# Kernel optimization log

Hardware: AMD Instinct MI355X
Metric: run time of the kernel (lower is better)

The kernel has to match this reference:

```python
import jax, jax.numpy as jnp
import numpy as np

E = 1024   # embed_dim
H = 16     # num_heads
D = E // H # head_dim = 64
HD2 = D // 2
B = 2
S = 2048


def setup_inputs() -> dict:
    key = jax.random.key(0)
    ks = jax.random.split(key, 12)
    def lin(k, fan_in, fan_out):
        # xavier-uniform-ish init, stored in [in, out] (jax) convention
        lim = float(np.sqrt(6.0 / (fan_in + fan_out)))
        return jax.random.uniform(k, (fan_in, fan_out), jnp.float32, -lim, lim)
    return {
        "query": jax.random.normal(ks[0], (B, S, E), jnp.float32),
        "xi_scale": jax.random.uniform(ks[1], (B,), jnp.float32),
        "Wq": lin(ks[2], E, E), "bq": jnp.zeros((E,), jnp.float32),
        "Wk": lin(ks[3], E, E), "bk": jnp.zeros((E,), jnp.float32),
        "Wv": lin(ks[4], E, E), "bv": jnp.zeros((E,), jnp.float32),
        "Wo": lin(ks[5], E, E), "bo": jnp.zeros((E,), jnp.float32),
        "enc_w1": lin(ks[6], 1, HD2), "enc_b1": jnp.zeros((HD2,), jnp.float32),
        "ln_g": jnp.ones((HD2,), jnp.float32), "ln_b": jnp.zeros((HD2,), jnp.float32),
        "enc_w2": lin(ks[7], HD2, D), "enc_b2": jnp.zeros((D,), jnp.float32),
        "scale_gating": jnp.ones((H,), jnp.float32),
    }


def reference(query, xi_scale, Wq, bq, Wk, bk, Wv, bv, Wo, bo,
              enc_w1, enc_b1, ln_g, ln_b, enc_w2, enc_b2, scale_gating):
    b, s, e = query.shape
    h, d = H, e // H
    # --- scale adaptation: xi -> Linear -> LayerNorm -> GELU -> Linear ---
    x = xi_scale[:, None] @ enc_w1 + enc_b1                  # [B, D/2]
    mu = x.mean(-1, keepdims=True)
    var = ((x - mu) ** 2).mean(-1, keepdims=True)
    x = (x - mu) / jnp.sqrt(var + 1e-5) * ln_g + ln_b
    x = jax.nn.gelu(x, approximate=False)
    xe = x @ enc_w2 + enc_b2                                 # [B, D]
    adapt = 1.0 + jax.nn.sigmoid(scale_gating)[None, :, None] * xe[:, None, :]  # [B, H, D]
    # --- projections (self-attention: key = value = query) ---
    q = (query @ Wq + bq).reshape(b, s, h, d).transpose(0, 2, 1, 3) * adapt[:, :, None, :]
    k = (query @ Wk + bk).reshape(b, s, h, d).transpose(0, 2, 1, 3) * adapt[:, :, None, :]
    v = (query @ Wv + bv).reshape(b, s, h, d).transpose(0, 2, 1, 3)
    # --- explicit QK^T / sqrt(d) -> softmax -> V ---
    inv_scale = 1.0 / float(np.sqrt(d))
    scores = jnp.einsum('bhqd,bhkd->bhqk', q, k) * inv_scale  # [B, H, S, S]
    attn = jax.nn.softmax(scores, axis=-1)
    out = jnp.einsum('bhqk,bhkd->bhqd', attn, v)              # [B, H, S, D]
    out = out.transpose(0, 2, 1, 3).reshape(b, s, e)
    return out @ Wo + bo
```

## Files before the change

### kernel.cpp

```cpp
#include <hip/hip_runtime.h>

typedef __bf16 bf16;
typedef __attribute__((ext_vector_type(8))) __bf16 bf16x8;
typedef __attribute__((ext_vector_type(4))) float f32x4;
typedef __attribute__((ext_vector_type(16))) float f32x16;
typedef unsigned int u32;

#define MFMA16(a, b, c) __builtin_amdgcn_mfma_f32_16x16x32_bf16((a), (b), (c), 0, 0, 0)
#define MFMA32(a, b, c) __builtin_amdgcn_mfma_f32_32x32x16_bf16((a), (b), (c), 0, 0, 0)

#define BB 2
#define SS 2048
#define EE 1024
#define HH 16
#define DD 64
#define MM (BB * SS)
#define NT (SS / 64)

__device__ inline f32x4 zero4() {
    f32x4 z; z.x = 0.f; z.y = 0.f; z.z = 0.f; z.w = 0.f; return z;
}

__device__ __forceinline__ void gload16(const bf16* g, bf16* l) {
    __builtin_amdgcn_global_load_lds(
        (const __attribute__((address_space(1))) u32*)(const void*)g,
        (__attribute__((address_space(3))) u32*)(void*)l,
        16, 0, 0);
}

__device__ __forceinline__ u32 pkbf(float a, float b) {
    union { __bf16 h; unsigned short s; } ua, ub;
    ua.h = (__bf16)a; ub.h = (__bf16)b;
    return (u32)ua.s | ((u32)ub.s << 16);
}

#define PSWAP(a, b) asm("v_permlane32_swap_b32 %0, %1" : "+v"(a), "+v"(b))

__global__ __launch_bounds__(256) void prep_kernel(
    const float* __restrict__ query, bf16* __restrict__ qc,
    const float* __restrict__ s0, const float* __restrict__ s1,
    const float* __restrict__ s2, const float* __restrict__ s3,
    bf16* __restrict__ d0, bf16* __restrict__ d1,
    bf16* __restrict__ d2, bf16* __restrict__ d3,
    const float* __restrict__ xi, const float* __restrict__ w1,
    const float* __restrict__ b1, const float* __restrict__ lng,
    const float* __restrict__ lnb, const float* __restrict__ w2,
    const float* __restrict__ b2, const float* __restrict__ gate,
    float* __restrict__ adapt) {
    __shared__ bf16 tile[64 * 72];
    const int bid = blockIdx.x;
    const int t = threadIdx.x;

    if (bid < 2048) {
        const int i = (bid * 256 + t) * 8;
        float4 a = *(const float4*)(query + i);
        float4 b = *(const float4*)(query + i + 4);
        bf16 tmp[8];
        tmp[0] = (bf16)a.x; tmp[1] = (bf16)a.y; tmp[2] = (bf16)a.z; tmp[3] = (bf16)a.w;
        tmp[4] = (bf16)b.x; tmp[5] = (bf16)b.y; tmp[6] = (bf16)b.z; tmp[7] = (bf16)b.w;
        *(uint4*)(qc + i) = *(uint4*)tmp;
    } else if (bid < 3072) {
        const int m = (bid - 2048) >> 8;
        const int idx0 = (bid - 2048) & 255;
        const float* W = (m == 0) ? s0 : (m == 1) ? s1 : (m == 2) ? s2 : s3;
        bf16* Wt = (m == 0) ? d0 : (m == 1) ? d1 : (m == 2) ? d2 : d3;
        const int k0 = (idx0 >> 4) * 64, n0 = (idx0 & 15) * 64;
#pragma unroll
        for (int i = 0; i < 2; ++i) {
            int idx = i * 256 + t;
            int r = idx >> 3, c = (idx & 7) * 8;
            float4 a = *(const float4*)(W + (k0 + r) * EE + n0 + c);
            float4 b = *(const float4*)(W + (k0 + r) * EE + n0 + c + 4);
            bf16 tmp[8];
            tmp[0] = (bf16)a.x; tmp[1] = (bf16)a.y; tmp[2] = (bf16)a.z; tmp[3] = (bf16)a.w;
            tmp[4] = (bf16)b.x; tmp[5] = (bf16)b.y; tmp[6] = (bf16)b.z; tmp[7] = (bf16)b.w;
            *(uint4*)(tile + r * 72 + c) = *(uint4*)tmp;
        }
        __syncthreads();
#pragma unroll
        for (int i = 0; i < 2; ++i) {
            int idx = i * 256 + t;
            int n = idx >> 3, kc = (idx & 7) * 8;
            bf16 tmp[8];
#pragma unroll
            for (int j = 0; j < 8; ++j) tmp[j] = tile[(kc + j) * 72 + n];
            *(uint4*)(Wt + (n0 + n) * EE + k0 + kc) = *(uint4*)tmp;
        }
    } else {
        const int b = bid - 3072;
        float* xs = (float*)tile;
        if (t < 64) {
            const float xiv = xi[b];
            float xv = 0.f;
            if (t < 32) xv = xiv * w1[t] + b1[t];
            float sm = xv;
            for (int off = 1; off < 32; off <<= 1) sm += __shfl_xor(sm, off);
            const float mu = sm * (1.f / 32.f);
            float dv = (t < 32) ? (xv - mu) : 0.f;
            float s2 = dv * dv;
            for (int off = 1; off < 32; off <<= 1) s2 += __shfl_xor(s2, off);
            const float var = s2 * (1.f / 32.f);
            if (t < 32) {
                float xn = (xv - mu) * rsqrtf(var + 1e-5f) * lng[t] + lnb[t];
                float ge = 0.5f * xn * (1.f + erff(xn * 0.70710678118654752f));
                xs[t] = ge;
            }
        }
        __syncthreads();
        if (t < 64) {
            float acc = b2[t];
            for (int j = 0; j < 32; ++j) acc += xs[j] * w2[j * DD + t];
            for (int h = 0; h < HH; ++h) {
                float sg = 1.f / (1.f + __expf(-gate[h]));
                adapt[(b * HH + h) * DD + t] = 1.f + sg * acc;
            }
        }
    }
}

__global__ __launch_bounds__(256, 3) void gemm_qkv(
    const bf16* __restrict__ Aq, const bf16* __restrict__ Bqk,
    const bf16* __restrict__ Av,
    const float* __restrict__ bias, const float* __restrict__ bias2,
    const float* __restrict__ bias3, const float* __restrict__ adapt,
    bf16* __restrict__ outqk, bf16* __restrict__ outvt) {
    __shared__ bf16 sh[16384];
    bf16* As = sh;
    bf16* Bs = sh + 8192;

    const int t = threadIdx.x;
    const int w = t >> 6, lane = t & 63;
    const int mrow = lane & 15, quad = lane >> 4;
    const int wm = (w & 1) * 64, wn = (w >> 1) * 64;

    int md, bx, by;
    const bf16 *Ap, *Bp;
    int bid = blockIdx.x;
    if (bid < 512) { md = 5; bx = bid & 31; by = bid >> 5; Ap = Aq; Bp = Bqk; }
    else { md = 4; bid -= 512; bx = bid & 7; by = bid >> 3; Ap = Av; Bp = Aq; }
    const int m0 = bx * 128, n0 = by * 128;
    const int m2 = (md == 5) ? (by >> 3) : 0;

    f32x4 acc[4][4];
#pragma unroll
    for (int i = 0; i < 4; ++i)
#pragma unroll
        for (int j = 0; j < 4; ++j) acc[i][j] = zero4();

    const int dr = lane >> 2;
    const int dcg = ((lane & 3) ^ (dr & 3)) * 8;
    const bf16* Ag = Ap + (size_t)(m0 + w * 16 + dr) * EE + dcg;
    const bf16* Bg = Bp + (size_t)(n0 + w * 16 + dr) * EE + dcg;
    bf16* Al = As + (w * 16) * 32;
    bf16* Bl = Bs + (w * 16) * 32;

    gload16(Ag, Al);
    gload16(Ag + 64 * EE, Al + 64 * 32);
    gload16(Bg, Bl);
    gload16(Bg + 64 * EE, Bl + 64 * 32);

    for (int kt = 0; kt < 32; ++kt) {
        __syncthreads();
        if (kt < 31) {
            const int kn = (kt + 1) * 32;
            const int nb = (kt + 1) & 1;
            gload16(Ag + kn, Al + nb * 4096);
            gload16(Ag + 64 * EE + kn, Al + nb * 4096 + 64 * 32);
            gload16(Bg + kn, Bl + nb * 4096);
            gload16(Bg + 64 * EE + kn, Bl + nb * 4096 + 64 * 32);
        }
        const bf16* Ab = As + (kt & 1) * 4096;
        const bf16* Bb = Bs + (kt & 1) * 4096;
        const int sw = (quad ^ (mrow & 3)) * 8;
        bf16x8 af[4], bfr[4];
#pragma unroll
        for (int i = 0; i < 4; ++i)
            af[i] = *(const bf16x8*)(Ab + (wm + i * 16 + mrow) * 32 + sw);
#pragma unroll
        for (int j = 0; j < 4; ++j)
            bfr[j] = *(const bf16x8*)(Bb + (wn + j * 16 + mrow) * 32 + sw);
#pragma unroll
        for (int i = 0; i < 4; ++i)
#pragma unroll
            for (int j = 0; j < 4; ++j)
                acc[i][j] = MFMA16(af[i], bfr[j], acc[i][j]);
    }

    __syncthreads();

    if (md == 5) {
        const int bq_ = m0 >> 11;
        float cmul[4], cadd[4];
#pragma unroll
        for (int j = 0; j < 4; ++j) {
            const int cl = (n0 & 1023) + wn + j * 16 + mrow;
            const int hh = cl >> 6, dd2 = cl & 63;
            const float ad = adapt[(bq_ * HH + hh) * DD + dd2];
            const float sc = m2 ? 1.f : 0.18033688011113811f;
            cmul[j] = ad * sc;
            cadd[j] = (m2 ? bias2[cl] : bias[cl]) * ad * sc;
        }
#pragma unroll
        for (int i = 0; i < 4; ++i)
#pragma unroll
            for (int j = 0; j < 4; ++j) {
                const int lcol = wn + j * 16 + mrow;
#pragma unroll
                for (int r = 0; r < 4; ++r) {
                    const int lrow = wm + i * 16 + quad * 4 + r;
                    const float v = acc[i][j][r] * cmul[j] + cadd[j];
                    *(bf16*)((char*)sh + lrow * 256 +
                             ((lcol * 2) ^ ((lrow & 15) << 4))) = (bf16)v;
                }
            }
    } else {
        float radd[16];
#pragma unroll
        for (int i = 0; i < 4; ++i)
#pragma unroll
            for (int r = 0; r < 4; ++r)
                radd[i * 4 + r] = bias3[m0 + wm + i * 16 + quad * 4 + r];
#pragma unroll
        for (int i = 0; i < 4; ++i)
#pragma unroll
            for (int j = 0; j < 4; ++j) {
                const int lcol = wn + j * 16 + mrow;
#pragma unroll
                for (int r = 0; r < 4; ++r) {
                    const int lrow = wm + i * 16 + quad * 4 + r;
                    const float v = acc[i][j][r] + radd[i * 4 + r];
                    *(bf16*)((char*)sh + lrow * 256 +
                             ((lcol * 2) ^ ((lrow & 15) << 4))) = (bf16)v;
                }
            }
    }
    __syncthreads();

#pragma unroll
    for (int p = 0; p < 8; ++p) {
        const int lrow = p * 16 + (t >> 4);
        const int lcol0 = (t & 15) * 8;
        bf16x8 val = *(const bf16x8*)((const char*)sh + lrow * 256 +
                                      ((lcol0 * 2) ^ ((lrow & 15) << 4)));
        if (md == 5) {
            const int bq_ = m0 >> 11;
            const int s_ = (m0 + lrow) & (SS - 1);
            const int cl = (n0 & 1023) + lcol0;
            const int hh = cl >> 6, d0 = cl & 63;
            if (!m2) {
                *(bf16x8*)(outqk + ((size_t)(bq_ * HH + hh) * SS + s_) * DD + d0) = val;
            } else {
                const size_t base = (size_t)MM * EE + (size_t)(bq_ * HH + hh) * 131072;
                const int a2 = (s_ >> 6) * 4096 + ((s_ >> 5) & 1) * 2048 +
                               (d0 >> 4) * 512 +
                               ((s_ & 31) + ((d0 >> 3) & 1) * 32) * 8;
                *(bf16x8*)(outqk + base + a2) = val;
            }
        } else {
            const int rowv = m0 + lrow;
            const int hv = rowv >> 6, dv = rowv & 63;
            const int colv = n0 + lcol0;
            const int bv_ = colv >> 11, sv = colv & (SS - 1);
            const size_t base = (size_t)(bv_ * HH + hv) * 131072;
            const int a2 = (sv >> 6) * 4096 + (dv >> 5) * 2048 +
                           ((sv >> 4) & 3) * 512 +
                           ((dv & 31) + ((sv >> 3) & 1) * 32) * 8;
            *(bf16x8*)(outvt + base + a2) = val;
        }
    }
}

__global__ __launch_bounds__(256, 3) void gemm_o(
    const bf16* __restrict__ A, const bf16* __restrict__ Bt,
    const float* __restrict__ bias, float* __restrict__ outf) {
    __shared__ bf16 As[2 * 128 * 64];
    __shared__ bf16 Bs[2 * 64 * 64];

    const int t = threadIdx.x;
    const int w = t >> 6, lane = t & 63;
    const int mrow = lane & 15, quad = lane >> 4;
    const int m0 = blockIdx.x * 128, n0 = blockIdx.y * 64;

    f32x4 acc[2][4];
#pragma unroll
    for (int i = 0; i < 2; ++i)
#pragma unroll
        for (int j = 0; j < 4; ++j) acc[i][j] = zero4();

    const int grow = lane >> 3;
    const int gsw = ((lane & 7) ^ grow) * 8;
    const bf16* Ag = A + (size_t)(m0 + w * 32 + grow) * EE + gsw;
    const bf16* Bg = Bt + (size_t)(n0 + w * 16 + grow) * EE + gsw;
    bf16* Al = As + (w * 32) * 64;
    bf16* Bl = Bs + (w * 16) * 64;

#pragma unroll
    for (int i = 0; i < 4; ++i) gload16(Ag + i * 8 * EE, Al + i * 8 * 64);
#pragma unroll
    for (int i = 0; i < 2; ++i) gload16(Bg + i * 8 * EE, Bl + i * 8 * 64);

    for (int kt = 0; kt < 16; ++kt) {
        __syncthreads();
        if (kt < 15) {
            const int kn = (kt + 1) * 64;
            const int nb = (kt + 1) & 1;
#pragma unroll
            for (int i = 0; i < 4; ++i)
                gload16(Ag + i * 8 * EE + kn, Al + nb * 8192 + i * 8 * 64);
#pragma unroll
            for (int i = 0; i < 2; ++i)
                gload16(Bg + i * 8 * EE + kn, Bl + nb * 4096 + i * 8 * 64);
        }
        const bf16* Ab = As + (kt & 1) * 8192;
        const bf16* Bb = Bs + (kt & 1) * 4096;
#pragma unroll
        for (int ks = 0; ks < 2; ++ks) {
            const int cg = ks * 4 + quad;
            const int sw = (cg ^ (mrow & 7)) * 8;
            bf16x8 af[2], bfr[4];
#pragma unroll
            for (int mi = 0; mi < 2; ++mi)
                af[mi] = *(const bf16x8*)(Ab + (w * 32 + mi * 16 + mrow) * 64 + sw);
#pragma unroll
            for (int nj = 0; nj < 4; ++nj)
                bfr[nj] = *(const bf16x8*)(Bb + (nj * 16 + mrow) * 64 + sw);
#pragma unroll
            for (int mi = 0; mi < 2; ++mi)
#pragma unroll
                for (int nj = 0; nj < 4; ++nj)
                    acc[mi][nj] = MFMA16(af[mi], bfr[nj], acc[mi][nj]);
        }
    }

    __syncthreads();
    char* fs = (char*)As;
    float cadd[4];
#pragma unroll
    for (int nj = 0; nj < 4; ++nj) cadd[nj] = bias[n0 + nj * 16 + mrow];
#pragma unroll
    for (int mi = 0; mi < 2; ++mi)
#pragma unroll
        for (int nj = 0; nj < 4; ++nj) {
            const int lcol = nj * 16 + mrow;
#pragma unroll
            for (int r = 0; r < 4; ++r) {
                const int lrow = w * 32 + mi * 16 + quad * 4 + r;
                *(float*)(fs + lrow * 256 + ((lcol * 4) ^ ((lrow & 15) << 4))) =
                    acc[mi][nj][r] + cadd[nj];
            }
        }
    __syncthreads();

#pragma unroll
    for (int p = 0; p < 8; ++p) {
        const int lrow = p * 16 + (t >> 4);
        const int lcol0 = (t & 15) * 4;
        float4 val = *(const float4*)(fs + lrow * 256 +
                                      ((lcol0 * 4) ^ ((lrow & 15) << 4)));
        *(float4*)(outf + (size_t)(m0 + lrow) * EE + n0 + lcol0) = val;
    }
}

#define ATTN_SMPACK(ST0, ST1, PBN)                                           \
    do {                                                                     \
        u32 P32_[2][8];                                                      \
        _Pragma("unroll")                                                    \
        for (int rp = 0; rp < 8; ++rp) {                                     \
            float pa_ = __builtin_amdgcn_exp2f((ST0)[2 * rp]);               \
            float pb_ = __builtin_amdgcn_exp2f((ST0)[2 * rp + 1]);           \
            ls[rp & 3] += pa_ + pb_;                                         \
            P32_[0][rp] = pkbf(pa_, pb_);                                    \
            float pc_ = __builtin_amdgcn_exp2f((ST1)[2 * rp]);               \
            float pd_ = __builtin_amdgcn_exp2f((ST1)[2 * rp + 1]);           \
            ls[rp & 3] += pc_ + pd_;                                         \
            P32_[1][rp] = pkbf(pc_, pd_);                                    \
        }                                                                    \
        _Pragma("unroll")                                                    \
        for (int c = 0; c < 4; ++c) {                                        \
            const int mfs_ = c >> 1, ro_ = (c & 1) * 4;                      \
            u32 a0_ = P32_[mfs_][ro_ + 0], a1_ = P32_[mfs_][ro_ + 1];        \
            u32 b0_ = P32_[mfs_][ro_ + 2], b1_ = P32_[mfs_][ro_ + 3];        \
            PSWAP(a0_, b0_); PSWAP(a1_, b1_);                                \
            PBN[c * 4 + 0] = a0_; PBN[c * 4 + 1] = a1_;                      \
            PBN[c * 4 + 2] = b0_; PBN[c * 4 + 3] = b1_;                      \
        }                                                                    \
    } while (0)

#define ATTN_STEP(T, KU, VFP, VFN, PBP, PBN, DOPF)                           \
    do {                                                                     \
        _Pragma("unroll")                                                    \
        for (int mf = 0; mf < 2; ++mf)                                       \
            _Pragma("unroll")                                                \
            for (int c = 0; c < 4; ++c)                                      \
                VFN[mf * 4 + c] = *(const bf16x8*)(vbase + (T) * 4096 +      \
                                                   mf * 2048 + c * 512);     \
        f32x16 st0, st1;                                                     \
        _Pragma("unroll")                                                    \
        for (int i = 0; i < 16; ++i) { st0[i] = 0.f; st1[i] = 0.f; }         \
        __builtin_amdgcn_s_setprio(1);                                       \
        _Pragma("unroll")                                                    \
        for (int c = 0; c < 4; ++c) {                                        \
            st0 = MFMA32(KU[c], qf[c], st0);                                 \
            st1 = MFMA32(KU[4 + c], qf[c], st1);                             \
            union { u32 u[4]; bf16x8 v; } pv_;                               \
            pv_.u[0] = PBP[c * 4 + 0]; pv_.u[1] = PBP[c * 4 + 1];            \
            pv_.u[2] = PBP[c * 4 + 2]; pv_.u[3] = PBP[c * 4 + 3];            \
            oacc[0] = MFMA32(VFP[c], pv_.v, oacc[0]);                        \
            oacc[1] = MFMA32(VFP[4 + c], pv_.v, oacc[1]);                    \
        }                                                                    \
        __builtin_amdgcn_s_setprio(0);                                       \
        if (DOPF) {                                                          \
            const int ktp_ = ((T) + 2 < NT) ? (T) + 2 : NT - 1;              \
            _Pragma("unroll")                                                \
            for (int mf = 0; mf < 2; ++mf)                                   \
                _Pragma("unroll")                                            \
                for (int c = 0; c < 4; ++c)                                  \
                    KU[mf * 4 + c] = *(const bf16x8*)(kbase + ktp_ * 4096 +  \
                                                      mf * 2048 + c * 512);  \
        }                                                                    \
        ATTN_SMPACK(st0, st1, PBN);                                          \
    } while (0)

__global__ __launch_bounds__(256, 2) void attn_kernel(
    const bf16* __restrict__ q, const bf16* __restrict__ k,
    const bf16* __restrict__ vt, bf16* __restrict__ o0) {
    __shared__ bf16 lds[4 * 2112];

    const int t = threadIdx.x;
    const int w = t >> 6, lane = t & 63;
    const int q32 = lane & 31, h = lane >> 5;
    const int bh = blockIdx.x & 31;
    const int qb = blockIdx.x >> 5;
    const int qr0 = qb * 128 + w * 32;

    bf16x8 qf[4];
#pragma unroll
    for (int c = 0; c < 4; ++c)
        qf[c] = *(const bf16x8*)(q + (size_t)(bh * SS + qr0 + q32) * DD + c * 16 + h * 8);

    const bf16* kbase = k + (size_t)bh * 131072 + lane * 8;
    const bf16* vbase = vt + (size_t)bh * 131072 + lane * 8;

    f32x16 oacc[2];
#pragma unroll
    for (int i = 0; i < 16; ++i) { oacc[0][i] = 0.f; oacc[1][i] = 0.f; }
    float ls[4] = {0.f, 0.f, 0.f, 0.f};

    bf16x8 Ka[8], Kb[8], vfA[8], vfB[8];
    u32 pbA[16], pbB[16];

#pragma unroll
    for (int mf = 0; mf < 2; ++mf)
#pragma unroll
        for (int c = 0; c < 4; ++c) {
            Ka[mf * 4 + c] = *(const bf16x8*)(kbase + mf * 2048 + c * 512);
            Kb[mf * 4 + c] = *(const bf16x8*)(kbase + 4096 + mf * 2048 + c * 512);
            vfA[mf * 4 + c] = *(const bf16x8*)(vbase + mf * 2048 + c * 512);
        }

    {
        f32x16 st0, st1;
#pragma unroll
        for (int i = 0; i < 16; ++i) { st0[i] = 0.f; st1[i] = 0.f; }
        __builtin_amdgcn_s_setprio(1);
#pragma unroll
        for (int c = 0; c < 4; ++c) {
            st0 = MFMA32(Ka[c], qf[c], st0);
            st1 = MFMA32(Ka[4 + c], qf[c], st1);
        }
        __builtin_amdgcn_s_setprio(0);
#pragma unroll
        for (int mf = 0; mf < 2; ++mf)
#pragma unroll
            for (int c = 0; c < 4; ++c)
                Ka[mf * 4 + c] = *(const bf16x8*)(kbase + 2 * 4096 + mf * 2048 + c * 512);
        ATTN_SMPACK(st0, st1, pbA);
    }

    for (int i = 0; i < 15; ++i) {
        ATTN_STEP(2 * i + 1, Kb, vfA, vfB, pbA, pbB, 1);
        ATTN_STEP(2 * i + 2, Ka, vfB, vfA, pbB, pbA, 1);
    }
    ATTN_STEP(31, Kb, vfA, vfB, pbA, pbB, 0);

    __builtin_amdgcn_s_setprio(1);
#pragma unroll
    for (int c = 0; c < 4; ++c) {
        union { u32 u[4]; bf16x8 v; } pv_;
        pv_.u[0] = pbB[c * 4 + 0]; pv_.u[1] = pbB[c * 4 + 1];
        pv_.u[2] = pbB[c * 4 + 2]; pv_.u[3] = pbB[c * 4 + 3];
        oacc[0] = MFMA32(vfB[c], pv_.v, oacc[0]);
        oacc[1] = MFMA32(vfB[4 + c], pv_.v, oacc[1]);
    }
    __builtin_amdgcn_s_setprio(0);

    float lsum = (ls[0] + ls[1]) + (ls[2] + ls[3]);
    lsum += __shfl_xor(lsum, 32);
    const float inv = 1.f / lsum;

    bf16* ob = lds + w * 2112;
#pragma unroll
    for (int mf = 0; mf < 2; ++mf)
#pragma unroll
        for (int rp = 0; rp < 8; ++rp) {
            const int d = 32 * mf + 2 * (rp & 1) + 8 * (rp >> 1) + 4 * h;
            *(u32*)(ob + q32 * 66 + d) =
                pkbf(oacc[mf][2 * rp] * inv, oacc[mf][2 * rp + 1] * inv);
        }
    __syncthreads();

    const int b = bh >> 4, head = bh & 15;
    const int half = lane & 1;
    const int r = lane >> 1;
#pragma unroll
    for (int i = 0; i < 4; ++i) {
        bf16x8 val = *(const bf16x8*)(ob + r * 66 + half * 32 + i * 8);
        *(bf16x8*)(o0 + (size_t)(b * SS + qr0 + r) * EE + head * DD +
                   half * 32 + i * 8) = val;
    }
}

extern "C" void kernel_launch(void* const* d_in, const int* in_sizes, int n_in,
                              void* d_out, int out_size, void* d_ws, size_t ws_size,
                              hipStream_t stream) {
    const float* query = (const float*)d_in[0];
    const float* xi    = (const float*)d_in[1];
    const float* Wq = (const float*)d_in[2];  const float* bq = (const float*)d_in[3];
    const float* Wk = (const float*)d_in[4];  const float* bk = (const float*)d_in[5];
    const float* Wv = (const float*)d_in[6];  const float* bv = (const float*)d_in[7];
    const float* Wo = (const float*)d_in[8];  const float* bo = (const float*)d_in[9];
    const float* ew1 = (const float*)d_in[10]; const float* eb1 = (const float*)d_in[11];
    const float* lng = (const float*)d_in[12]; const float* lnb = (const float*)d_in[13];
    const float* ew2 = (const float*)d_in[14]; const float* eb2 = (const float*)d_in[15];
    const float* gate = (const float*)d_in[16];
    float* out = (float*)d_out;

    char* ws = (char*)d_ws;
    const size_t SZ = (size_t)MM * EE * sizeof(bf16);
    const size_t WSZ = (size_t)EE * EE * sizeof(bf16);

    bf16* queryc = (bf16*)(ws);
    bf16* p0     = (bf16*)(ws);
    bf16* qws    = (bf16*)(ws + SZ);
    bf16* kws    = (bf16*)(ws + 2 * SZ);
    bf16* vtws   = (bf16*)(ws + 3 * SZ);
    bf16* wqT    = (bf16*)(ws + 4 * SZ);
    bf16* wkT    = (bf16*)(ws + 4 * SZ + WSZ);
    bf16* wvT    = (bf16*)(ws + 4 * SZ + 2 * WSZ);
    bf16* woT    = (bf16*)(ws + 4 * SZ + 3 * WSZ);
    float* adaptws = (float*)(ws + 4 * SZ + 4 * WSZ);

    prep_kernel<<<3074, 256, 0, stream>>>(query, queryc, Wq, Wk, Wv, Wo,
                                          wqT, wkT, wvT, woT,
                                          xi, ew1, eb1, lng, lnb, ew2, eb2, gate,
                                          adaptws);

    gemm_qkv<<<768, 256, 0, stream>>>(queryc, wqT, wvT, bq, bk, bv, adaptws,
                                      qws, vtws);

    attn_kernel<<<512, 256, 0, stream>>>(qws, kws, vtws, p0);

    gemm_o<<<dim3(MM / 128, EE / 64), 256, 0, stream>>>(p0, woT, bo, out);
}
```

Before: 206.7 us.

## Split attention key range across two wave groups and merge partials via LDS

Each attention block now has 512 threads. The upper four waves process the second half of the key tiles, and the lower four waves process the first half, each group looping over 16 tiles instead of 32. The upper group writes its unnormalised output accumulators and row sums to LDS (now a float buffer). The lower group adds them in, normalises and stores. The goal is to double the waves in flight and halve each wave's serial key loop, at the cost of extra LDS traffic, barriers and a tighter launch bound (512,4) that may force register spilling.

```diff
diff --git a/kernel.cpp b/kernel.cpp
--- a/kernel.cpp
+++ b/kernel.cpp
@@ -15,7 +15,7 @@
 #define HH 16
 #define DD 64
 #define MM (BB * SS)
-#define NT (SS / 64)
+#define NT2 16
 
 __device__ inline f32x4 zero4() {
     f32x4 z; z.x = 0.f; z.y = 0.f; z.z = 0.f; z.w = 0.f; return z;
@@ -410,7 +410,7 @@
         }                                                                    \
         __builtin_amdgcn_s_setprio(0);                                       \
         if (DOPF) {                                                          \
-            const int ktp_ = ((T) + 2 < NT) ? (T) + 2 : NT - 1;              \
+            const int ktp_ = ((T) + 2 < NT2) ? (T) + 2 : NT2 - 1;            \
             _Pragma("unroll")                                                \
             for (int mf = 0; mf < 2; ++mf)                                   \
                 _Pragma("unroll")                                            \
@@ -421,25 +421,27 @@
         ATTN_SMPACK(st0, st1, PBN);                                          \
     } while (0)
 
-__global__ __launch_bounds__(256, 2) void attn_kernel(
+__global__ __launch_bounds__(512, 4) void attn_kernel(
     const bf16* __restrict__ q, const bf16* __restrict__ k,
     const bf16* __restrict__ vt, bf16* __restrict__ o0) {
-    __shared__ bf16 lds[4 * 2112];
+    __shared__ float ldsf[4 * 2112];
 
     const int t = threadIdx.x;
     const int w = t >> 6, lane = t & 63;
     const int q32 = lane & 31, h = lane >> 5;
+    const int wq = w & 3;
+    const int kh = w >> 2;
     const int bh = blockIdx.x & 31;
     const int qb = blockIdx.x >> 5;
-    const int qr0 = qb * 128 + w * 32;
+    const int qr0 = qb * 128 + wq * 32;
 
     bf16x8 qf[4];
 #pragma unroll
     for (int c = 0; c < 4; ++c)
         qf[c] = *(const bf16x8*)(q + (size_t)(bh * SS + qr0 + q32) * DD + c * 16 + h * 8);
 
-    const bf16* kbase = k + (size_t)bh * 131072 + lane * 8;
-    const bf16* vbase = vt + (size_t)bh * 131072 + lane * 8;
+    const bf16* kbase = k + (size_t)bh * 131072 + (size_t)kh * NT2 * 4096 + lane * 8;
+    const bf16* vbase = vt + (size_t)bh * 131072 + (size_t)kh * NT2 * 4096 + lane * 8;
 
     f32x16 oacc[2];
 #pragma unroll
@@ -477,11 +479,11 @@
         ATTN_SMPACK(st0, st1, pbA);
     }
 
-    for (int i = 0; i < 15; ++i) {
+    for (int i = 0; i < NT2 / 2 - 1; ++i) {
         ATTN_STEP(2 * i + 1, Kb, vfA, vfB, pbA, pbB, 1);
         ATTN_STEP(2 * i + 2, Ka, vfB, vfA, pbB, pbA, 1);
     }
-    ATTN_STEP(31, Kb, vfA, vfB, pbA, pbB, 0);
+    ATTN_STEP(NT2 - 1, Kb, vfA, vfB, pbA, pbB, 0);
 
     __builtin_amdgcn_s_setprio(1);
 #pragma unroll
@@ -496,27 +498,53 @@
 
     float lsum = (ls[0] + ls[1]) + (ls[2] + ls[3]);
     lsum += __shfl_xor(lsum, 32);
-    const float inv = 1.f / lsum;
-
-    bf16* ob = lds + w * 2112;
-#pragma unroll
-    for (int mf = 0; mf < 2; ++mf)
-#pragma unroll
-        for (int rp = 0; rp < 8; ++rp) {
-            const int d = 32 * mf + 2 * (rp & 1) + 8 * (rp >> 1) + 4 * h;
-            *(u32*)(ob + q32 * 66 + d) =
-                pkbf(oacc[mf][2 * rp] * inv, oacc[mf][2 * rp + 1] * inv);
-        }
-    __syncthreads();
-
-    const int b = bh >> 4, head = bh & 15;
-    const int half = lane & 1;
-    const int r = lane >> 1;
-#pragma unroll
-    for (int i = 0; i < 4; ++i) {
-        bf16x8 val = *(const bf16x8*)(ob + r * 66 + half * 32 + i * 8);
-        *(bf16x8*)(o0 + (size_t)(b * SS + qr0 + r) * EE + head * DD +
-                   half * 32 + i * 8) = val;
+
+    if (kh) {
+        float* cb = ldsf + wq * 2112;
+#pragma unroll
+        for (int i = 0; i < 16; ++i) {
+            cb[i * 64 + lane] = oacc[0][i];
+            cb[(16 + i) * 64 + lane] = oacc[1][i];
+        }
+        cb[32 * 64 + lane] = lsum;
+    }
+    __syncthreads();
+    float inv = 0.f;
+    if (!kh) {
+        const float* cb = ldsf + wq * 2112;
+#pragma unroll
+        for (int i = 0; i < 16; ++i) {
+            oacc[0][i] += cb[i * 64 + lane];
+            oacc[1][i] += cb[(16 + i) * 64 + lane];
+        }
+        lsum += cb[32 * 64 + lane];
+        inv = 1.f / lsum;
+    }
+    __syncthreads();
+
+    bf16* ob = (bf16*)ldsf + wq * 2112;
+    if (!kh) {
+#pragma unroll
+        for (int mf = 0; mf < 2; ++mf)
+#pragma unroll
+            for (int rp = 0; rp < 8; ++rp) {
+                const int d = 32 * mf + 2 * (rp & 1) + 8 * (rp >> 1) + 4 * h;
+                *(u32*)(ob + q32 * 66 + d) =
+                    pkbf(oacc[mf][2 * rp] * inv, oacc[mf][2 * rp + 1] * inv);
+            }
+    }
+    __syncthreads();
+
+    if (!kh) {
+        const int b = bh >> 4, head = bh & 15;
+        const int hf = lane & 1;
+        const int r = lane >> 1;
+#pragma unroll
+        for (int i = 0; i < 4; ++i) {
+            bf16x8 val = *(const bf16x8*)(ob + r * 66 + hf * 32 + i * 8);
+            *(bf16x8*)(o0 + (size_t)(b * SS + qr0 + r) * EE + head * DD +
+                       hf * 32 + i * 8) = val;
+        }
     }
 }
 
@@ -558,7 +586,7 @@
     gemm_qkv<<<768, 256, 0, stream>>>(queryc, wqT, wvT, bq, bk, bv, adaptws,
                                       qws, vtws);
 
-    attn_kernel<<<512, 256, 0, stream>>>(qws, kws, vtws, p0);
+    attn_kernel<<<512, 512, 0, stream>>>(qws, kws, vtws, p0);
 
     gemm_o<<<dim3(MM / 128, EE / 64), 256, 0, stream>>>(p0, woT, bo, out);
 }
```

Measured after the change: 454.4 us. 2.2x slower.
